# Kernel tuning notes

Hardware: AMD Instinct MI355X
Metric: run time of the kernel (lower is better)

Reference implementation:

```python
import jax, jax.numpy as jnp
import numpy as np
from math import sqrt

B, N, M, HID, NH = 16, 512, 1024, 512, 8
HS = HID // NH  # 64


def layer_norm(x, g, b, eps=1e-5):
    mu = jnp.mean(x, axis=-1, keepdims=True)
    var = jnp.var(x, axis=-1, keepdims=True)
    return (x - mu) * jax.lax.rsqrt(var + eps) * g + b


def apply_moverz(x, s, c):
    # x: [B, L, NH, HS]; s, c: [B, L, 1, HS//2]
    x0, x1 = x[..., 0::2], x[..., 1::2]
    return jnp.concatenate([x0 * c - x1 * s, x1 * c + x0 * s], axis=-1)


def attention(q, k, v, mask):
    # q: [B,Nq,NH,HS], k/v: [B,Nk,NH,HS], mask broadcastable to [B,NH,Nq,Nk]
    attn = jnp.einsum('bnhd,bmhd->bhnm', q, k) / sqrt(HS)
    attn = jnp.where(mask, -jnp.inf, attn)
    attn = jax.nn.softmax(attn, axis=-1)
    x = jnp.einsum('bhnm,bmhd->bnhd', attn, v)
    return x.reshape(x.shape[0], x.shape[1], HID)


def setup_inputs() -> dict:
    key = jax.random.key(0)
    ks = jax.random.split(key, 24)
    inp = {}
    inp['tgt'] = jax.random.normal(ks[0], (B, N, HID), dtype=jnp.float32)
    inp['mem'] = jax.random.normal(ks[1], (B, M, HID), dtype=jnp.float32)
    th_p = jax.random.uniform(ks[2], (B, N, 1, HS // 2), dtype=jnp.float32) * (2 * np.pi)
    th_k = jax.random.uniform(ks[3], (B, M, 1, HS // 2), dtype=jnp.float32) * (2 * np.pi)
    inp['pep_mass_sin'] = jnp.sin(th_p)
    inp['pep_mass_cos'] = jnp.cos(th_p)
    inp['peaks_moverz_sin'] = jnp.sin(th_k)
    inp['peaks_moverz_cos'] = jnp.cos(th_k)
    # causal self-attn mask (True = masked)
    inp['tgt_mask'] = jnp.triu(jnp.ones((N, N), dtype=bool), k=1)[None, None]
    # pad last 64 memory positions
    pad = jnp.arange(M) >= (M - 64)
    inp['mem_key_padding_mask'] = jnp.broadcast_to(pad[None, None, None, :], (B, 1, 1, M))
    s = 0.02
    w = lambda i, shape: jax.random.normal(ks[i], shape, dtype=jnp.float32) * s
    # MaskedMultiHeadAttn params
    inp['mmha_w'] = w(4, (3 * HID, HID)); inp['mmha_b'] = jnp.zeros((3 * HID,), jnp.float32)
    inp['mmha_ow'] = w(5, (HID, HID)); inp['mmha_ob'] = jnp.zeros((HID,), jnp.float32)
    inp['mmha_g'] = jnp.ones((HID,), jnp.float32); inp['mmha_beta'] = jnp.zeros((HID,), jnp.float32)
    # MultiHeadAttn (cross) params
    inp['mha_qw'] = w(6, (HID, HID)); inp['mha_qb'] = jnp.zeros((HID,), jnp.float32)
    inp['mha_kvw'] = w(7, (2 * HID, HID)); inp['mha_kvb'] = jnp.zeros((2 * HID,), jnp.float32)
    inp['mha_ow'] = w(8, (HID, HID)); inp['mha_ob'] = jnp.zeros((HID,), jnp.float32)
    inp['mha_g'] = jnp.ones((HID,), jnp.float32); inp['mha_beta'] = jnp.zeros((HID,), jnp.float32)
    # FFN params (no bias)
    inp['ffn_w1'] = w(9, (4 * HID, HID))
    inp['ffn_w2'] = w(10, (HID, 4 * HID))
    inp['ffn_g'] = jnp.ones((HID,), jnp.float32); inp['ffn_beta'] = jnp.zeros((HID,), jnp.float32)
    return inp


def reference(tgt, mem, pep_mass_sin, pep_mass_cos, peaks_moverz_sin, peaks_moverz_cos,
              tgt_mask, mem_key_padding_mask,
              mmha_w, mmha_b, mmha_ow, mmha_ob, mmha_g, mmha_beta,
              mha_qw, mha_qb, mha_kvw, mha_kvb, mha_ow, mha_ob, mha_g, mha_beta,
              ffn_w1, ffn_w2, ffn_g, ffn_beta):
    # --- masked self-attention ---
    qkv = (tgt @ mmha_w.T + mmha_b).reshape(B, N, NH, 3 * HS)
    q, k, v = jnp.split(qkv, 3, axis=-1)
    x = attention(q, k, v, tgt_mask)
    tgt = layer_norm(x @ mmha_ow.T + mmha_ob + tgt, mmha_g, mmha_beta)
    # --- cross-attention with moverz distance bias ---
    q = (tgt @ mha_qw.T + mha_qb).reshape(B, N, NH, HS)
    q = apply_moverz(q, pep_mass_sin, pep_mass_cos)
    kv = (mem @ mha_kvw.T + mha_kvb).reshape(B, M, NH, 2 * HS)
    k, v = jnp.split(kv, 2, axis=-1)
    k = apply_moverz(k, peaks_moverz_sin, peaks_moverz_cos)
    x = attention(q, k, v, mem_key_padding_mask)
    tgt = layer_norm(x @ mha_ow.T + mha_ob + tgt, mha_g, mha_beta)
    # --- FFN ---
    h = jax.nn.relu(tgt @ ffn_w1.T) @ ffn_w2.T
    tgt = layer_norm(tgt + h, ffn_g, ffn_beta)
    return tgt
```

## Files before the change

kernel.cpp:

```cpp
#include <hip/hip_runtime.h>
#include <hip/hip_bf16.h>

#define BB 16
#define NN 512
#define MM 1024
#define HIDD 512
#define NHH 8

typedef unsigned short ushort_t;
typedef __attribute__((ext_vector_type(8))) short short8;
typedef __attribute__((ext_vector_type(8))) _Float16 half8;
typedef __attribute__((ext_vector_type(4))) _Float16 half4;
typedef __attribute__((ext_vector_type(2))) __fp16 fp16x2;
typedef __attribute__((ext_vector_type(4))) float f32x4;

__device__ __forceinline__ ushort_t f2bf(float x) {
    unsigned u = __float_as_uint(x);
    u += 0x7fff + ((u >> 16) & 1);
    return (ushort_t)(u >> 16);
}

#define GLD16(g, l) __builtin_amdgcn_global_load_lds(                      \
    (const __attribute__((address_space(1))) void*)(g),                    \
    (__attribute__((address_space(3))) void*)(l), 16, 0, 0)


__device__ __forceinline__ void xcd_swizzle(int& colb, int& rowb) {
    int id = blockIdx.x + blockIdx.y * gridDim.x;
    int C = gridDim.x;
    int xcd = id & 7;
    int slot = id >> 3;
    int rows_per = gridDim.y >> 3;
    colb = slot % C;
    rowb = xcd * rows_per + slot / C;
}

__device__ __forceinline__ void xcd_swz_p(int id, int C, int Rdiv8,
                                          int& colb, int& rowb) {
    int xcd = id & 7;
    int slot = id >> 3;
    colb = slot % C;
    rowb = xcd * Rdiv8 + slot / C;
}

__global__ __launch_bounds__(256)
void gemm_bf(const ushort_t* __restrict__ A, const ushort_t* __restrict__ W,
             const float* __restrict__ bias, float* __restrict__ C,
             ushort_t* __restrict__ Cb, _Float16* __restrict__ Ch,
             int K, int Cout, int relu) {
    __shared__ __align__(16) ushort_t smem[2][8192];
    const int tid = threadIdx.x;
    const int lane = tid & 63;
    const int wid = tid >> 6;
    const int wm = wid >> 1, wn = wid & 1;
    int colb, rowb;
    xcd_swizzle(colb, rowb);
    const long row0 = (long)rowb * 128;
    const long col0 = (long)colb * 128;

    const int sr = lane >> 2;
    const int skq = lane & 3;
    const int skx = skq ^ ((sr >> 1) & 3);
    const ushort_t* Ag = A + (row0 + wid * 32 + sr) * (long)K + skx * 8;
    const ushort_t* Wg = W + (col0 + wid * 32 + sr) * (long)K + skx * 8;
    const int sa0 = (wid * 32) * 32, sa1 = (wid * 32 + 16) * 32;

    f32x4 acc[4][4] = {};
    const int lr = lane & 15;
    const int kg = lane >> 4;
    const int kgx = (kg ^ ((lr >> 1) & 3)) * 8;

    GLD16(Ag, &smem[0][sa0]);
    GLD16(Ag + 16 * (long)K, &smem[0][sa1]);
    GLD16(Wg, &smem[0][4096 + sa0]);
    GLD16(Wg + 16 * (long)K, &smem[0][4096 + sa1]);

    int pb = 0;
    for (int k0 = 0; k0 < K; k0 += 32, pb ^= 1) {
        __syncthreads();
        int kn = k0 + 32;
        if (kn < K) {
            GLD16(Ag + kn, &smem[pb ^ 1][sa0]);
            GLD16(Ag + 16 * (long)K + kn, &smem[pb ^ 1][sa1]);
            GLD16(Wg + kn, &smem[pb ^ 1][4096 + sa0]);
            GLD16(Wg + 16 * (long)K + kn, &smem[pb ^ 1][4096 + sa1]);
        }
        const ushort_t* Ab = smem[pb];
        const ushort_t* Wb = smem[pb] + 4096;
        short8 af[4], bfr[4];
#pragma unroll
        for (int i = 0; i < 4; i++)
            af[i] = *(const short8*)&Ab[(wm * 64 + i * 16 + lr) * 32 + kgx];
#pragma unroll
        for (int j = 0; j < 4; j++)
            bfr[j] = *(const short8*)&Wb[(wn * 64 + j * 16 + lr) * 32 + kgx];
#pragma unroll
        for (int i = 0; i < 4; i++)
#pragma unroll
            for (int j = 0; j < 4; j++)
                acc[i][j] = __builtin_amdgcn_mfma_f32_16x16x32_bf16(
                    af[i], bfr[j], acc[i][j], 0, 0, 0);
    }

#pragma unroll
    for (int i = 0; i < 4; i++) {
#pragma unroll
        for (int j = 0; j < 4; j++) {
            long row = row0 + wm * 64 + i * 16 + kg * 4;
            long col = col0 + wn * 64 + j * 16 + lr;
            float bv = bias ? bias[col] : 0.f;
#pragma unroll
            for (int r = 0; r < 4; r++) {
                float x = acc[i][j][r] + bv;
                if (relu) x = fmaxf(x, 0.f);
                size_t idx = (row + r) * (size_t)Cout + col;
                if (Ch)      Ch[idx] = (_Float16)x;
                else if (Cb) Cb[idx] = f2bf(x);
                else         C[idx] = x;
            }
        }
    }
}

__global__ __launch_bounds__(256)
void gemm_qkv_kv(const ushort_t* __restrict__ A, const ushort_t* __restrict__ Wq,
                 const float* __restrict__ bq, _Float16* __restrict__ qkvh,
                 const ushort_t* __restrict__ Mem, const ushort_t* __restrict__ Wkv,
                 const float* __restrict__ bkv,
                 const float* __restrict__ sn, const float* __restrict__ cs,
                 _Float16* __restrict__ Krot, _Float16* __restrict__ Vth) {
    __shared__ __align__(16) ushort_t smem[2][8192];
    const int tid = threadIdx.x;
    const int lane = tid & 63;
    const int wid = tid >> 6;
    const int lr = lane & 15;
    const int kg = lane >> 4;
    const int sr = lane >> 2;
    const int skq = lane & 3;
    const int skx = skq ^ ((sr >> 1) & 3);
    const int kgx = (kg ^ ((lr >> 1) & 3)) * 8;
    const int K = 512;

    if (blockIdx.x < 768) {
        int colb, rowb;
        xcd_swz_p(blockIdx.x, 12, 8, colb, rowb);
        const long row0 = (long)rowb * 128;
        const long col0 = (long)colb * 128;
        const int wm = wid >> 1, wn = wid & 1;
        const ushort_t* Ag = A + (row0 + wid * 32 + sr) * (long)K + skx * 8;
        const ushort_t* Wg = Wq + (col0 + wid * 32 + sr) * (long)K + skx * 8;
        const int sa0 = (wid * 32) * 32, sa1 = (wid * 32 + 16) * 32;

        f32x4 acc[4][4] = {};
        GLD16(Ag, &smem[0][sa0]);
        GLD16(Ag + 16 * (long)K, &smem[0][sa1]);
        GLD16(Wg, &smem[0][4096 + sa0]);
        GLD16(Wg + 16 * (long)K, &smem[0][4096 + sa1]);

        int pb = 0;
        for (int k0 = 0; k0 < K; k0 += 32, pb ^= 1) {
            __syncthreads();
            int kn = k0 + 32;
            if (kn < K) {
                GLD16(Ag + kn, &smem[pb ^ 1][sa0]);
                GLD16(Ag + 16 * (long)K + kn, &smem[pb ^ 1][sa1]);
                GLD16(Wg + kn, &smem[pb ^ 1][4096 + sa0]);
                GLD16(Wg + 16 * (long)K + kn, &smem[pb ^ 1][4096 + sa1]);
            }
            const ushort_t* Ab = smem[pb];
            const ushort_t* Wb = smem[pb] + 4096;
            short8 af[4], bfr[4];
#pragma unroll
            for (int i = 0; i < 4; i++)
                af[i] = *(const short8*)&Ab[(wm * 64 + i * 16 + lr) * 32 + kgx];
#pragma unroll
            for (int j = 0; j < 4; j++)
                bfr[j] = *(const short8*)&Wb[(wn * 64 + j * 16 + lr) * 32 + kgx];
#pragma unroll
            for (int i = 0; i < 4; i++)
#pragma unroll
                for (int j = 0; j < 4; j++)
                    acc[i][j] = __builtin_amdgcn_mfma_f32_16x16x32_bf16(
                        af[i], bfr[j], acc[i][j], 0, 0, 0);
        }

#pragma unroll
        for (int i = 0; i < 4; i++)
#pragma unroll
            for (int j = 0; j < 4; j++) {
                long row = row0 + wm * 64 + i * 16 + kg * 4;
                long col = col0 + wn * 64 + j * 16 + lr;
                float bv = bq[col];
#pragma unroll
                for (int r = 0; r < 4; r++)
                    qkvh[(row + r) * (size_t)1536 + col] =
                        (_Float16)(acc[i][j][r] + bv);
            }
    } else {
        _Float16* Cs = (_Float16*)smem;
        int colb, rowb;
        xcd_swz_p(blockIdx.x - 768, 8, 16, colb, rowb);
        const long row0 = (long)rowb * 128;
        const int h = colb;
        const long col0 = (long)h * 128;
        const int wm = wid >> 1, wn = wid & 1;
        const ushort_t* Ag = Mem + (row0 + wid * 32 + sr) * (long)K + skx * 8;
        const ushort_t* Wg = Wkv + (col0 + wid * 32 + sr) * (long)K + skx * 8;
        const int sa0 = (wid * 32) * 32, sa1 = (wid * 32 + 16) * 32;

        f32x4 acc[4][4] = {};
        GLD16(Ag, &smem[0][sa0]);
        GLD16(Ag + 16 * (long)K, &smem[0][sa1]);
        GLD16(Wg, &smem[0][4096 + sa0]);
        GLD16(Wg + 16 * (long)K, &smem[0][4096 + sa1]);

        int pb = 0;
        for (int k0 = 0; k0 < K; k0 += 32, pb ^= 1) {
            __syncthreads();
            int kn = k0 + 32;
            if (kn < K) {
                GLD16(Ag + kn, &smem[pb ^ 1][sa0]);
                GLD16(Ag + 16 * (long)K + kn, &smem[pb ^ 1][sa1]);
                GLD16(Wg + kn, &smem[pb ^ 1][4096 + sa0]);
                GLD16(Wg + 16 * (long)K + kn, &smem[pb ^ 1][4096 + sa1]);
            }
            const ushort_t* Ab = smem[pb];
            const ushort_t* Wb = smem[pb] + 4096;
            short8 af[4], bfr[4];
#pragma unroll
            for (int i = 0; i < 4; i++)
                af[i] = *(const short8*)&Ab[(wm * 64 + i * 16 + lr) * 32 + kgx];
#pragma unroll
            for (int j = 0; j < 4; j++)
                bfr[j] = *(const short8*)&Wb[(wn * 64 + j * 16 + lr) * 32 + kgx];
#pragma unroll
            for (int i = 0; i < 4; i++)
#pragma unroll
                for (int j = 0; j < 4; j++)
                    acc[i][j] = __builtin_amdgcn_mfma_f32_16x16x32_bf16(
                        af[i], bfr[j], acc[i][j], 0, 0, 0);
        }

        const int b_ = (int)(row0 >> 10);
        const int m0_ = (int)(row0 & 1023);
#pragma unroll
        for (int half = 0; half < 2; half++) {
            __syncthreads();
            if (wn == half) {
#pragma unroll
                for (int i = 0; i < 4; i++)
#pragma unroll
                    for (int j = 0; j < 4; j++) {
                        int row = wm * 64 + i * 16 + kg * 4;
                        int col = j * 16 + lr;
                        float bv = bkv[col0 + half * 64 + col];
#pragma unroll
                        for (int r = 0; r < 4; r++)
                            Cs[(row + r) * 76 + col] = (_Float16)(acc[i][j][r] + bv);
                    }
            }
            __syncthreads();
            if (half == 0) {
                for (int idx = tid; idx < 4096; idx += 256) {
                    int rr = idx >> 5, j = idx & 31;
                    size_t srow = (size_t)row0 + rr;
                    float x0 = (float)Cs[rr * 76 + 2 * j];
                    float x1 = (float)Cs[rr * 76 + 2 * j + 1];
                    float s = sn[srow * 32 + j], c = cs[srow * 32 + j];
                    Krot[srow * 512 + h * 64 + j]      = (_Float16)(x0 * c - x1 * s);
                    Krot[srow * 512 + h * 64 + 32 + j] = (_Float16)(x1 * c + x0 * s);
                }
            } else {
                for (int idx = tid; idx < 1024; idx += 256) {
                    int d = idx >> 4, c = idx & 15;
                    half8 v;
#pragma unroll
                    for (int k = 0; k < 8; k++) v[k] = Cs[(c * 8 + k) * 76 + d];
                    *(half8*)(Vth + (((size_t)(b_ * NHH + h)) * 64 + d) * MM
                              + m0_ + c * 8) = v;
                }
            }
        }
    }
}

__global__ __launch_bounds__(256)
void gemm_bf64(const ushort_t* __restrict__ A, const ushort_t* __restrict__ W,
               const float* __restrict__ bias, float* __restrict__ C,
               ushort_t* __restrict__ Cb, _Float16* __restrict__ Ch,
               int K, int Cout, int relu) {
    __shared__ __align__(16) ushort_t smem[2][6144];
    const int tid = threadIdx.x;
    const int lane = tid & 63;
    const int w = tid >> 6;
    int colb, rowb;
    xcd_swizzle(colb, rowb);
    const long row0 = (long)rowb * 128;
    const long col0 = (long)colb * 64;

    const int sr = lane >> 2;
    const int skq = lane & 3;
    const int skx = skq ^ ((sr >> 1) & 3);
    const ushort_t* Ag = A + (row0 + w * 32 + sr) * (long)K + skx * 8;
    const ushort_t* Wg = W + (col0 + w * 16 + sr) * (long)K + skx * 8;
    const int sa0 = (w * 32) * 32, sa1 = (w * 32 + 16) * 32;
    const int sw0 = 4096 + (w * 16) * 32;

    f32x4 acc[2][4] = {};
    const int lr = lane & 15;
    const int kg = lane >> 4;
    const int kgx = (kg ^ ((lr >> 1) & 3)) * 8;

    GLD16(Ag, &smem[0][sa0]);
    GLD16(Ag + 16 * (long)K, &smem[0][sa1]);
    GLD16(Wg, &smem[0][sw0]);

    int pb = 0;
    for (int k0 = 0; k0 < K; k0 += 32, pb ^= 1) {
        __syncthreads();
        int kn = k0 + 32;
        if (kn < K) {
            GLD16(Ag + kn, &smem[pb ^ 1][sa0]);
            GLD16(Ag + 16 * (long)K + kn, &smem[pb ^ 1][sa1]);
            GLD16(Wg + kn, &smem[pb ^ 1][sw0]);
        }
        const ushort_t* Ab = smem[pb];
        const ushort_t* Wb = smem[pb] + 4096;
        short8 af[2], bfr[4];
#pragma unroll
        for (int i = 0; i < 2; i++)
            af[i] = *(const short8*)&Ab[(w * 32 + i * 16 + lr) * 32 + kgx];
#pragma unroll
        for (int j = 0; j < 4; j++)
            bfr[j] = *(const short8*)&Wb[(j * 16 + lr) * 32 + kgx];
#pragma unroll
        for (int i = 0; i < 2; i++)
#pragma unroll
            for (int j = 0; j < 4; j++)
                acc[i][j] = __builtin_amdgcn_mfma_f32_16x16x32_bf16(
                    af[i], bfr[j], acc[i][j], 0, 0, 0);
    }

#pragma unroll
    for (int i = 0; i < 2; i++) {
#pragma unroll
        for (int j = 0; j < 4; j++) {
            long row = row0 + w * 32 + i * 16 + kg * 4;
            long col = col0 + j * 16 + lr;
            float bv = bias ? bias[col] : 0.f;
#pragma unroll
            for (int r = 0; r < 4; r++) {
                float x = acc[i][j][r] + bv;
                if (relu) x = fmaxf(x, 0.f);
                size_t idx = (row + r) * (size_t)Cout + col;
                if (Ch)      Ch[idx] = (_Float16)x;
                else if (Cb) Cb[idx] = f2bf(x);
                else         C[idx] = x;
            }
        }
    }
}

__global__ __launch_bounds__(256)
void gemm_bf64_sk(const ushort_t* __restrict__ A, const ushort_t* __restrict__ W,
                  int lda, int Kslice, float* __restrict__ C0,
                  float* __restrict__ C1, int Cout) {
    __shared__ __align__(16) ushort_t smem[2][6144];
    const int tid = threadIdx.x;
    const int lane = tid & 63;
    const int w = tid >> 6;
    int colb, rowb;
    xcd_swizzle(colb, rowb);
    const long row0 = (long)rowb * 128;
    const long col0 = (long)colb * 64;
    const long koff = (long)blockIdx.z * Kslice;
    float* __restrict__ C = blockIdx.z ? C1 : C0;

    const int sr = lane >> 2;
    const int skq = lane & 3;
    const int skx = skq ^ ((sr >> 1) & 3);
    const ushort_t* Ag = A + (row0 + w * 32 + sr) * (long)lda + koff + skx * 8;
    const ushort_t* Wg = W + (col0 + w * 16 + sr) * (long)lda + koff + skx * 8;
    const int sa0 = (w * 32) * 32, sa1 = (w * 32 + 16) * 32;
    const int sw0 = 4096 + (w * 16) * 32;

    f32x4 acc[2][4] = {};
    const int lr = lane & 15;
    const int kg = lane >> 4;
    const int kgx = (kg ^ ((lr >> 1) & 3)) * 8;

    GLD16(Ag, &smem[0][sa0]);
    GLD16(Ag + 16 * (long)lda, &smem[0][sa1]);
    GLD16(Wg, &smem[0][sw0]);

    int pb = 0;
    for (int k0 = 0; k0 < Kslice; k0 += 32, pb ^= 1) {
        __syncthreads();
        int kn = k0 + 32;
        if (kn < Kslice) {
            GLD16(Ag + kn, &smem[pb ^ 1][sa0]);
            GLD16(Ag + 16 * (long)lda + kn, &smem[pb ^ 1][sa1]);
            GLD16(Wg + kn, &smem[pb ^ 1][sw0]);
        }
        const ushort_t* Ab = smem[pb];
        const ushort_t* Wb = smem[pb] + 4096;
        short8 af[2], bfr[4];
#pragma unroll
        for (int i = 0; i < 2; i++)
            af[i] = *(const short8*)&Ab[(w * 32 + i * 16 + lr) * 32 + kgx];
#pragma unroll
        for (int j = 0; j < 4; j++)
            bfr[j] = *(const short8*)&Wb[(j * 16 + lr) * 32 + kgx];
#pragma unroll
        for (int i = 0; i < 2; i++)
#pragma unroll
            for (int j = 0; j < 4; j++)
                acc[i][j] = __builtin_amdgcn_mfma_f32_16x16x32_bf16(
                    af[i], bfr[j], acc[i][j], 0, 0, 0);
    }

#pragma unroll
    for (int i = 0; i < 2; i++)
#pragma unroll
        for (int j = 0; j < 4; j++) {
            long row = row0 + w * 32 + i * 16 + kg * 4;
            long col = col0 + j * 16 + lr;
#pragma unroll
            for (int r = 0; r < 4; r++)
                C[(row + r) * (size_t)Cout + col] = acc[i][j][r];
        }
}

__global__ __launch_bounds__(256)
void gemm_q_rot(const ushort_t* __restrict__ A, const ushort_t* __restrict__ W,
                const float* __restrict__ bias,
                const float* __restrict__ sn, const float* __restrict__ cs,
                _Float16* __restrict__ Qrot) {
    __shared__ __align__(16) ushort_t smem[2][6144];
    _Float16* Cs = (_Float16*)smem;
    const int K = 512;
    const int tid = threadIdx.x;
    const int lane = tid & 63;
    const int w = tid >> 6;
    int colb, rowb;
    xcd_swizzle(colb, rowb);
    const long row0 = (long)rowb * 128;
    const int h = colb;
    const long col0 = (long)h * 64;

    const int sr = lane >> 2;
    const int skq = lane & 3;
    const int skx = skq ^ ((sr >> 1) & 3);
    const ushort_t* Ag = A + (row0 + w * 32 + sr) * (long)K + skx * 8;
    const ushort_t* Wg = W + (col0 + w * 16 + sr) * (long)K + skx * 8;
    const int sa0 = (w * 32) * 32, sa1 = (w * 32 + 16) * 32;
    const int sw0 = 4096 + (w * 16) * 32;

    f32x4 acc[2][4] = {};
    const int lr = lane & 15;
    const int kg = lane >> 4;
    const int kgx = (kg ^ ((lr >> 1) & 3)) * 8;

    GLD16(Ag, &smem[0][sa0]);
    GLD16(Ag + 16 * (long)K, &smem[0][sa1]);
    GLD16(Wg, &smem[0][sw0]);

    int pb = 0;
    for (int k0 = 0; k0 < K; k0 += 32, pb ^= 1) {
        __syncthreads();
        int kn = k0 + 32;
        if (kn < K) {
            GLD16(Ag + kn, &smem[pb ^ 1][sa0]);
            GLD16(Ag + 16 * (long)K + kn, &smem[pb ^ 1][sa1]);
            GLD16(Wg + kn, &smem[pb ^ 1][sw0]);
        }
        const ushort_t* Ab = smem[pb];
        const ushort_t* Wb = smem[pb] + 4096;
        short8 af[2], bfr[4];
#pragma unroll
        for (int i = 0; i < 2; i++)
            af[i] = *(const short8*)&Ab[(w * 32 + i * 16 + lr) * 32 + kgx];
#pragma unroll
        for (int j = 0; j < 4; j++)
            bfr[j] = *(const short8*)&Wb[(j * 16 + lr) * 32 + kgx];
#pragma unroll
        for (int i = 0; i < 2; i++)
#pragma unroll
            for (int j = 0; j < 4; j++)
                acc[i][j] = __builtin_amdgcn_mfma_f32_16x16x32_bf16(
                    af[i], bfr[j], acc[i][j], 0, 0, 0);
    }

    __syncthreads();
#pragma unroll
    for (int i = 0; i < 2; i++)
#pragma unroll
        for (int j = 0; j < 4; j++) {
            int row = w * 32 + i * 16 + kg * 4;
            int col = j * 16 + lr;
            float bv = bias[col0 + col];
#pragma unroll
            for (int r = 0; r < 4; r++)
                Cs[(row + r) * 76 + col] = (_Float16)(acc[i][j][r] + bv);
        }
    __syncthreads();
    for (int idx = tid; idx < 4096; idx += 256) {
        int rr = idx >> 5, j = idx & 31;
        size_t srow = (size_t)row0 + rr;
        float x0 = (float)Cs[rr * 76 + 2 * j], x1 = (float)Cs[rr * 76 + 2 * j + 1];
        float s = sn[srow * 32 + j], c = cs[srow * 32 + j];
        Qrot[srow * 512 + h * 64 + j]      = (_Float16)(x0 * c - x1 * s);
        Qrot[srow * 512 + h * 64 + 32 + j] = (_Float16)(x1 * c + x0 * s);
    }
}

__global__ __launch_bounds__(256)
void cvt_all(const float* __restrict__ tgt, const float* __restrict__ mem,
             const float* __restrict__ w0, const float* __restrict__ w1,
             const float* __restrict__ w2, const float* __restrict__ w3,
             const float* __restrict__ w4, const float* __restrict__ w5,
             const float* __restrict__ w6,
             ushort_t* __restrict__ Abf, ushort_t* __restrict__ membf,
             ushort_t* __restrict__ Wbf) {
    int blk = blockIdx.x;
    const float* src;
    ushort_t* dst;
    size_t off;
    if (blk < 4096)       { src = tgt; dst = Abf;   off = (size_t)blk * 1024; }
    else if (blk < 12288) { src = mem; dst = membf; off = (size_t)(blk - 4096) * 1024; }
    else {
        int wb = blk - 12288;
        dst = Wbf + (size_t)wb * 1024;
        if (wb < 768)       { src = w0; off = (size_t)wb * 1024; }
        else if (wb < 1024) { src = w1; off = (size_t)(wb - 768) * 1024; }
        else if (wb < 1280) { src = w2; off = (size_t)(wb - 1024) * 1024; }
        else if (wb < 1792) { src = w3; off = (size_t)(wb - 1280) * 1024; }
        else if (wb < 2048) { src = w4; off = (size_t)(wb - 1792) * 1024; }
        else if (wb < 3072) { src = w5; off = (size_t)(wb - 2048) * 1024; }
        else                { src = w6; off = (size_t)(wb - 3072) * 1024; }
        float4 v = *(const float4*)(src + off + threadIdx.x * 4);
        ushort4 o;
        o.x = f2bf(v.x); o.y = f2bf(v.y); o.z = f2bf(v.z); o.w = f2bf(v.w);
        *(ushort4*)(dst + threadIdx.x * 4) = o;
        return;
    }
    float4 v = *(const float4*)(src + off + threadIdx.x * 4);
    ushort4 o;
    o.x = f2bf(v.x); o.y = f2bf(v.y); o.z = f2bf(v.z); o.w = f2bf(v.w);
    *(ushort4*)(dst + off + threadIdx.x * 4) = o;
}

__global__ __launch_bounds__(256)
void prep_vt(const _Float16* __restrict__ src, int L, int stride,
             int hmul, int hadd, _Float16* __restrict__ Vt) {
    const int b = blockIdx.z, h = blockIdx.y, m0 = blockIdx.x * 64;
    const int tid = threadIdx.x;
    __shared__ _Float16 vt[64][72];
    for (int idx = tid; idx < 512; idx += 256) {
        int m = idx >> 3, c = idx & 7;
        half8 v = *(const half8*)(src + ((size_t)(b * L + m0 + m)) * stride
                                  + h * hmul + hadd + c * 8);
#pragma unroll
        for (int k = 0; k < 8; k++) vt[c * 8 + k][m] = v[k];
    }
    __syncthreads();
    for (int idx = tid; idx < 512; idx += 256) {
        int d = idx >> 3, c = idx & 7;
        *(half8*)(Vt + (((size_t)(b * NHH + h)) * 64 + d) * L + m0 + c * 8)
            = *(const half8*)&vt[d][c * 8];
    }
}

__global__ __launch_bounds__(256, 4)
void attn11(const _Float16* __restrict__ Q, int qstride, int qmul, int qadd,
            const _Float16* __restrict__ K, int kstride, int kmul, int kadd,
            const _Float16* __restrict__ Vt, int LV, int Lrows,
            ushort_t* __restrict__ out, int kvlen, int causal) {
    const int g = blockIdx.x;
    const int bh = (g & 7) * 16 + ((g >> 3) & 15);
    const int qraw = g >> 7;
    const int qb = causal ? ((0x12476530u >> (qraw << 2)) & 7) : qraw;
    const int b = bh >> 3, h = bh & 7;
    const int n0 = qb * 64;
    const int tid = threadIdx.x, lane = tid & 63, w = tid >> 6;
    const int quad = lane >> 4, l16 = lane & 15;
    const int qw = n0 + w * 16;

    __shared__ _Float16 Ks[2][64 * 64];
    __shared__ _Float16 Vs[2][64 * 64];
    __shared__ _Float16 Ps[4][16 * 64];
    _Float16* Pw = Ps[w];

    half8 bq[2];
#pragma unroll
    for (int c = 0; c < 2; c++)
        bq[c] = *(const half8*)(Q + ((size_t)(b * NN + qw + l16)) * qstride
                                + h * qmul + qadd + c * 32 + quad * 8);

    f32x4 acc[4] = {};
    float mrun = -3e38f, lrun = 0.f;

    const int srow = tid >> 3;
    const int scol = tid & 7;
    const int ssw = (scol ^ (srow & 7)) * 8;

    const int limit = causal ? (n0 + 64) : kvlen;
    const int nt = limit >> 6;

    const size_t kbase = ((size_t)(b * Lrows)) * kstride + h * kmul + kadd;
    const size_t vbase = (((size_t)(b * NHH + h)) * 64 + srow) * (size_t)LV;

    half8 kr0, kr1, vr0, vr1;
    {
        size_t kb = kbase + (size_t)srow * kstride + scol * 8;
        kr0 = *(const half8*)(K + kb);
        kr1 = *(const half8*)(K + kb + (size_t)32 * kstride);
        vr0 = *(const half8*)(Vt + vbase + scol * 8);
        vr1 = *(const half8*)(Vt + vbase + (size_t)32 * LV + scol * 8);
    }
    *(half8*)&Ks[0][srow * 64 + ssw] = kr0;
    *(half8*)&Ks[0][(srow + 32) * 64 + ssw] = kr1;
    *(half8*)&Vs[0][srow * 64 + ssw] = vr0;
    *(half8*)&Vs[0][(srow + 32) * 64 + ssw] = vr1;
    if (nt > 1) {
        size_t kb = kbase + (size_t)(64 + srow) * kstride + scol * 8;
        kr0 = *(const half8*)(K + kb);
        kr1 = *(const half8*)(K + kb + (size_t)32 * kstride);
        vr0 = *(const half8*)(Vt + vbase + 64 + scol * 8);
        vr1 = *(const half8*)(Vt + vbase + (size_t)32 * LV + 64 + scol * 8);
    }

    const float SC = 0.125f * 1.44269504f;
    const int fsw = l16 & 7;
    int pb = 0;
    for (int t = 0; t < nt; t++, pb ^= 1) {
        const int key0 = t * 64;
        __syncthreads();
        if (t + 1 < nt) {
            *(half8*)&Ks[pb ^ 1][srow * 64 + ssw] = kr0;
            *(half8*)&Ks[pb ^ 1][(srow + 32) * 64 + ssw] = kr1;
            *(half8*)&Vs[pb ^ 1][srow * 64 + ssw] = vr0;
            *(half8*)&Vs[pb ^ 1][(srow + 32) * 64 + ssw] = vr1;
            if (t + 2 < nt) {
                size_t kb = kbase + (size_t)((t + 2) * 64 + srow) * kstride + scol * 8;
                kr0 = *(const half8*)(K + kb);
                kr1 = *(const half8*)(K + kb + (size_t)32 * kstride);
                vr0 = *(const half8*)(Vt + vbase + (t + 2) * 64 + scol * 8);
                vr1 = *(const half8*)(Vt + vbase + (size_t)32 * LV
                                      + (t + 2) * 64 + scol * 8);
            }
        }

        const _Float16* Kb = Ks[pb];
        const _Float16* Vb = Vs[pb];
        f32x4 st[4];
        __builtin_amdgcn_s_setprio(1);
#pragma unroll
        for (int kt = 0; kt < 4; kt++) {
            const int rk = kt * 16 + l16;
            half8 ak0 = *(const half8*)&Kb[rk * 64 + ((quad ^ fsw) * 8)];
            half8 ak1 = *(const half8*)&Kb[rk * 64 + (((quad + 4) ^ fsw) * 8)];
            f32x4 z = {};
            z = __builtin_amdgcn_mfma_f32_16x16x32_f16(ak0, bq[0], z, 0, 0, 0);
            z = __builtin_amdgcn_mfma_f32_16x16x32_f16(ak1, bq[1], z, 0, 0, 0);
            st[kt] = z;
        }
        __builtin_amdgcn_s_setprio(0);

        if (causal && key0 + 64 > qw) {
            const int qabs = qw + l16;
#pragma unroll
            for (int kt = 0; kt < 4; kt++)
#pragma unroll
                for (int r = 0; r < 4; r++)
                    if (key0 + kt * 16 + quad * 4 + r > qabs)
                        st[kt][r] = -3e38f;
        }

        float plm = -3e38f;
#pragma unroll
        for (int kt = 0; kt < 4; kt++)
            plm = fmaxf(plm, fmaxf(fmaxf(st[kt][0], st[kt][1]),
                                   fmaxf(st[kt][2], st[kt][3])));

        const int keep = __all(plm - mrun <= 64.f);
        if (!keep) {
            float lm = fmaxf(plm, __shfl_xor(plm, 16));
            lm = fmaxf(lm, __shfl_xor(lm, 32));
            float mnew = fmaxf(mrun, lm);
            float corr = exp2f((mrun - mnew) * SC);
            mrun = mnew;
            lrun *= corr;
            float cb0 = __shfl(corr, (lane & 48) | (quad * 4 + 0));
            float cb1 = __shfl(corr, (lane & 48) | (quad * 4 + 1));
            float cb2 = __shfl(corr, (lane & 48) | (quad * 4 + 2));
            float cb3 = __shfl(corr, (lane & 48) | (quad * 4 + 3));
#pragma unroll
            for (int dt = 0; dt < 4; dt++) {
                acc[dt][0] *= cb0; acc[dt][1] *= cb1;
                acc[dt][2] *= cb2; acc[dt][3] *= cb3;
            }
        }
        const float mb = mrun * SC;
#pragma unroll
        for (int kt = 0; kt < 4; kt++) {
            float p0 = exp2f(__builtin_fmaf(st[kt][0], SC, -mb));
            float p1 = exp2f(__builtin_fmaf(st[kt][1], SC, -mb));
            float p2 = exp2f(__builtin_fmaf(st[kt][2], SC, -mb));
            float p3 = exp2f(__builtin_fmaf(st[kt][3], SC, -mb));
            lrun += (p0 + p1) + (p2 + p3);
            fp16x2 lo = __builtin_amdgcn_cvt_pkrtz(p0, p1);
            fp16x2 hi = __builtin_amdgcn_cvt_pkrtz(p2, p3);
            union { unsigned u[2]; half4 h; } pk;
            pk.u[0] = __builtin_bit_cast(unsigned, lo);
            pk.u[1] = __builtin_bit_cast(unsigned, hi);
            int jc = 2 * kt + (quad >> 1);
            *(half4*)&Pw[l16 * 64 + ((jc ^ fsw) * 8) + (quad & 1) * 4] = pk.h;
        }
        half8 ap[2];
#pragma unroll
        for (int c = 0; c < 2; c++)
            ap[c] = *(const half8*)&Pw[l16 * 64 + (((c * 4 + quad) ^ fsw) * 8)];
        __builtin_amdgcn_s_setprio(1);
#pragma unroll
        for (int dt = 0; dt < 4; dt++) {
            const int rv = dt * 16 + l16;
            half8 bv0 = *(const half8*)&Vb[rv * 64 + ((quad ^ fsw) * 8)];
            half8 bv1 = *(const half8*)&Vb[rv * 64 + (((quad + 4) ^ fsw) * 8)];
            acc[dt] = __builtin_amdgcn_mfma_f32_16x16x32_f16(ap[0], bv0, acc[dt], 0, 0, 0);
            acc[dt] = __builtin_amdgcn_mfma_f32_16x16x32_f16(ap[1], bv1, acc[dt], 0, 0, 0);
        }
        __builtin_amdgcn_s_setprio(0);
    }

    lrun += __shfl_xor(lrun, 16);
    lrun += __shfl_xor(lrun, 32);
    float invq = 1.f / lrun;
    float iv0 = __shfl(invq, (lane & 48) | (quad * 4 + 0));
    float iv1 = __shfl(invq, (lane & 48) | (quad * 4 + 1));
    float iv2 = __shfl(invq, (lane & 48) | (quad * 4 + 2));
    float iv3 = __shfl(invq, (lane & 48) | (quad * 4 + 3));
#pragma unroll
    for (int dt = 0; dt < 4; dt++) {
        size_t base = ((size_t)(b * NN + qw + quad * 4)) * 512
                      + h * 64 + dt * 16 + l16;
        out[base]           = f2bf(acc[dt][0] * iv0);
        out[base + 512]     = f2bf(acc[dt][1] * iv1);
        out[base + 1024]    = f2bf(acc[dt][2] * iv2);
        out[base + 1536]    = f2bf(acc[dt][3] * iv3);
    }
}

__global__ __launch_bounds__(256)
void ln_residual(const float* __restrict__ u, const float* __restrict__ u2,
                 const float* __restrict__ res,
                 const float* __restrict__ g, const float* __restrict__ be,
                 float* __restrict__ out, ushort_t* __restrict__ outbf) {
    const int row = blockIdx.x, t = threadIdx.x;
    const float* rp = res + (size_t)row * HIDD;
    const float* up = u + (size_t)row * HIDD;
    float z0 = rp[t] + up[t];
    float z1 = rp[t + 256] + up[t + 256];
    if (u2) {
        const float* up2 = u2 + (size_t)row * HIDD;
        z0 += up2[t];
        z1 += up2[t + 256];
    }
    float sm = z0 + z1, s2 = z0 * z0 + z1 * z1;
#pragma unroll
    for (int off = 1; off < 64; off <<= 1) {
        sm += __shfl_xor(sm, off, 64);
        s2 += __shfl_xor(s2, off, 64);
    }
    __shared__ float ps[4], ps2[4];
    int w = t >> 6;
    if ((t & 63) == 0) { ps[w] = sm; ps2[w] = s2; }
    __syncthreads();
    sm = ps[0] + ps[1] + ps[2] + ps[3];
    s2 = ps2[0] + ps2[1] + ps2[2] + ps2[3];
    float mu = sm * (1.f / 512.f);
    float var = s2 * (1.f / 512.f) - mu * mu;
    float rstd = rsqrtf(var + 1e-5f);
    float y0 = (z0 - mu) * rstd * g[t] + be[t];
    float y1 = (z1 - mu) * rstd * g[t + 256] + be[t + 256];
    out[(size_t)row * HIDD + t]       = y0;
    out[(size_t)row * HIDD + t + 256] = y1;
    if (outbf) {
        outbf[(size_t)row * HIDD + t]       = f2bf(y0);
        outbf[(size_t)row * HIDD + t + 256] = f2bf(y1);
    }
}

extern "C" void kernel_launch(void* const* d_in, const int* in_sizes, int n_in,
                              void* d_out, int out_size, void* d_ws, size_t ws_size,
                              hipStream_t stream) {
    const float* tgt      = (const float*)d_in[0];
    const float* mem      = (const float*)d_in[1];
    const float* pep_sin  = (const float*)d_in[2];
    const float* pep_cos  = (const float*)d_in[3];
    const float* pk_sin   = (const float*)d_in[4];
    const float* pk_cos   = (const float*)d_in[5];
    const float* mmha_w   = (const float*)d_in[8];
    const float* mmha_b   = (const float*)d_in[9];
    const float* mmha_ow  = (const float*)d_in[10];
    const float* mmha_ob  = (const float*)d_in[11];
    const float* mmha_g   = (const float*)d_in[12];
    const float* mmha_be  = (const float*)d_in[13];
    const float* mha_qw   = (const float*)d_in[14];
    const float* mha_qb   = (const float*)d_in[15];
    const float* mha_kvw  = (const float*)d_in[16];
    const float* mha_kvb  = (const float*)d_in[17];
    const float* mha_ow   = (const float*)d_in[18];
    const float* mha_ob   = (const float*)d_in[19];
    const float* mha_g    = (const float*)d_in[20];
    const float* mha_be   = (const float*)d_in[21];
    const float* ffn_w1   = (const float*)d_in[22];
    const float* ffn_w2   = (const float*)d_in[23];
    const float* ffn_g    = (const float*)d_in[24];
    const float* ffn_be   = (const float*)d_in[25];

    float* ws = (float*)d_ws;
    float* utmp  = ws;
    float* tgt12 = ws + 4194304;
    _Float16* hp = (_Float16*)(ws + 8388608);
    _Float16* qkvh  = hp;
    _Float16* Qrot  = hp + 12582912;
    _Float16* Vth   = hp + 16777216;
    _Float16* Krot  = hp + 25165824;
    ushort_t* membf = (ushort_t*)(hp + 33554432);
    ushort_t* Abf   = (ushort_t*)(hp + 41943040);
    ushort_t* Wbf   = (ushort_t*)(hp + 46137344);
    ushort_t* w_mmha = Wbf;
    ushort_t* w_mmow = Wbf + 786432;
    ushort_t* w_qw   = Wbf + 1048576;
    ushort_t* w_kvw  = Wbf + 1310720;
    ushort_t* w_mow  = Wbf + 1835008;
    ushort_t* w_f1   = Wbf + 2097152;
    ushort_t* w_f2   = Wbf + 3145728;
    _Float16* Vth_self = hp + 50331648;
    ushort_t* hbf = (ushort_t*)qkvh;
    float* utmp2 = (float*)Krot;
    float* out = (float*)d_out;
    (void)in_sizes; (void)n_in; (void)out_size; (void)ws_size;

    cvt_all<<<16384, 256, 0, stream>>>(tgt, mem, mmha_w, mmha_ow, mha_qw,
                                       mha_kvw, mha_ow, ffn_w1, ffn_w2,
                                       Abf, membf, Wbf);
    gemm_qkv_kv<<<1792, 256, 0, stream>>>(Abf, w_mmha, mmha_b, qkvh,
                                          membf, w_kvw, mha_kvb,
                                          pk_sin, pk_cos, Krot, Vth);
    prep_vt<<<dim3(8, NHH, BB), 256, 0, stream>>>(qkvh, NN, 1536, 192, 128, Vth_self);
    attn11<<<1024, 256, 0, stream>>>(qkvh, 1536, 192, 0, qkvh, 1536, 192, 64,
                                     Vth_self, NN, NN, Abf, 0, 1);
    gemm_bf64<<<dim3(8, 64), 256, 0, stream>>>(Abf, w_mmow, mmha_ob, utmp, nullptr, nullptr, 512, 512, 0);
    ln_residual<<<8192, 256, 0, stream>>>(utmp, nullptr, tgt, mmha_g, mmha_be, tgt12, Abf);
    gemm_q_rot<<<dim3(8, 64), 256, 0, stream>>>(Abf, w_qw, mha_qb, pep_sin, pep_cos, Qrot);
    attn11<<<1024, 256, 0, stream>>>(Qrot, 512, 64, 0, Krot, 512, 64, 0,
                                     Vth, MM, MM, Abf, MM - 64, 0);
    gemm_bf64<<<dim3(8, 64), 256, 0, stream>>>(Abf, w_mow, mha_ob, utmp, nullptr, nullptr, 512, 512, 0);
    ln_residual<<<8192, 256, 0, stream>>>(utmp, nullptr, tgt12, mha_g, mha_be, tgt12, Abf);
    gemm_bf<<<dim3(16, 64), 256, 0, stream>>>(Abf, w_f1, nullptr, nullptr, hbf, nullptr, 512, 2048, 1);
    gemm_bf64_sk<<<dim3(8, 64, 2), 256, 0, stream>>>(hbf, w_f2, 2048, 1024, utmp, utmp2, 512);
    ln_residual<<<8192, 256, 0, stream>>>(utmp, utmp2, tgt12, ffn_g, ffn_be, out, nullptr);
}
```

Before: 397.0 us.

## Triple-buffer LDS in GEMM kernels with explicit vmcnt-based waits

Every GEMM main loop moves from a double-buffered shared-memory pipeline to a three-stage ring. Each stage prefetches two K-tiles ahead and replaces `__syncthreads` with an inline `s_waitcnt vmcnt(N)` plus `s_barrier`, so one tile's loads stay in flight while the current tile is computed. The goal is to hide more global-to-LDS latency behind the MFMA work. The cost is 50% more shared memory per block, which may reduce occupancy. Near the end of the loop, redundant clamped loads are issued. In `gemm_q_rot` and the KV branch these pending loads are not explicitly drained before the shared buffer is reused, which may race.

```diff
diff --git a/kernel.cpp b/kernel.cpp
--- a/kernel.cpp
+++ b/kernel.cpp
@@ -23,6 +23,7 @@
 #define GLD16(g, l) __builtin_amdgcn_global_load_lds(                      \
     (const __attribute__((address_space(1))) void*)(g),                    \
     (__attribute__((address_space(3))) void*)(l), 16, 0, 0)
+
 
 
 __device__ __forceinline__ void xcd_swizzle(int& colb, int& rowb) {
@@ -48,7 +49,7 @@
              const float* __restrict__ bias, float* __restrict__ C,
              ushort_t* __restrict__ Cb, _Float16* __restrict__ Ch,
              int K, int Cout, int relu) {
-    __shared__ __align__(16) ushort_t smem[2][8192];
+    __shared__ __align__(16) ushort_t smem[3][8192];
     const int tid = threadIdx.x;
     const int lane = tid & 63;
     const int wid = tid >> 6;
@@ -70,23 +71,31 @@
     const int kg = lane >> 4;
     const int kgx = (kg ^ ((lr >> 1) & 3)) * 8;
 
+    const int nt = K >> 5;
     GLD16(Ag, &smem[0][sa0]);
     GLD16(Ag + 16 * (long)K, &smem[0][sa1]);
     GLD16(Wg, &smem[0][4096 + sa0]);
     GLD16(Wg + 16 * (long)K, &smem[0][4096 + sa1]);
-
-    int pb = 0;
-    for (int k0 = 0; k0 < K; k0 += 32, pb ^= 1) {
-        __syncthreads();
-        int kn = k0 + 32;
-        if (kn < K) {
-            GLD16(Ag + kn, &smem[pb ^ 1][sa0]);
-            GLD16(Ag + 16 * (long)K + kn, &smem[pb ^ 1][sa1]);
-            GLD16(Wg + kn, &smem[pb ^ 1][4096 + sa0]);
-            GLD16(Wg + 16 * (long)K + kn, &smem[pb ^ 1][4096 + sa1]);
-        }
-        const ushort_t* Ab = smem[pb];
-        const ushort_t* Wb = smem[pb] + 4096;
+    GLD16(Ag + 32, &smem[1][sa0]);
+    GLD16(Ag + 16 * (long)K + 32, &smem[1][sa1]);
+    GLD16(Wg + 32, &smem[1][4096 + sa0]);
+    GLD16(Wg + 16 * (long)K + 32, &smem[1][4096 + sa1]);
+
+    int cur = 0;
+    for (int t = 0; t < nt; t++) {
+        asm volatile("s_waitcnt vmcnt(4)\n\ts_barrier" ::: "memory");
+        __builtin_amdgcn_sched_barrier(0);
+        {
+            int nxt = (t + 2 < nt) ? t + 2 : nt - 1;
+            int nb = cur + 2; if (nb >= 3) nb -= 3;
+            long kk = (long)nxt << 5;
+            GLD16(Ag + kk, &smem[nb][sa0]);
+            GLD16(Ag + 16 * (long)K + kk, &smem[nb][sa1]);
+            GLD16(Wg + kk, &smem[nb][4096 + sa0]);
+            GLD16(Wg + 16 * (long)K + kk, &smem[nb][4096 + sa1]);
+        }
+        const ushort_t* Ab = smem[cur];
+        const ushort_t* Wb = smem[cur] + 4096;
         short8 af[4], bfr[4];
 #pragma unroll
         for (int i = 0; i < 4; i++)
@@ -100,7 +109,9 @@
             for (int j = 0; j < 4; j++)
                 acc[i][j] = __builtin_amdgcn_mfma_f32_16x16x32_bf16(
                     af[i], bfr[j], acc[i][j], 0, 0, 0);
-    }
+        cur = (cur == 2) ? 0 : cur + 1;
+    }
+    asm volatile("s_waitcnt vmcnt(0)" ::: "memory");
 
 #pragma unroll
     for (int i = 0; i < 4; i++) {
@@ -129,7 +140,7 @@
                  const float* __restrict__ bkv,
                  const float* __restrict__ sn, const float* __restrict__ cs,
                  _Float16* __restrict__ Krot, _Float16* __restrict__ Vth) {
-    __shared__ __align__(16) ushort_t smem[2][8192];
+    __shared__ __align__(16) ushort_t smem[3][8192];
     const int tid = threadIdx.x;
     const int lane = tid & 63;
     const int wid = tid >> 6;
@@ -140,6 +151,7 @@
     const int skx = skq ^ ((sr >> 1) & 3);
     const int kgx = (kg ^ ((lr >> 1) & 3)) * 8;
     const int K = 512;
+    const int nt = 16;
 
     if (blockIdx.x < 768) {
         int colb, rowb;
@@ -156,19 +168,26 @@
         GLD16(Ag + 16 * (long)K, &smem[0][sa1]);
         GLD16(Wg, &smem[0][4096 + sa0]);
         GLD16(Wg + 16 * (long)K, &smem[0][4096 + sa1]);
-
-        int pb = 0;
-        for (int k0 = 0; k0 < K; k0 += 32, pb ^= 1) {
-            __syncthreads();
-            int kn = k0 + 32;
-            if (kn < K) {
-                GLD16(Ag + kn, &smem[pb ^ 1][sa0]);
-                GLD16(Ag + 16 * (long)K + kn, &smem[pb ^ 1][sa1]);
-                GLD16(Wg + kn, &smem[pb ^ 1][4096 + sa0]);
-                GLD16(Wg + 16 * (long)K + kn, &smem[pb ^ 1][4096 + sa1]);
+        GLD16(Ag + 32, &smem[1][sa0]);
+        GLD16(Ag + 16 * (long)K + 32, &smem[1][sa1]);
+        GLD16(Wg + 32, &smem[1][4096 + sa0]);
+        GLD16(Wg + 16 * (long)K + 32, &smem[1][4096 + sa1]);
+
+        int cur = 0;
+        for (int t = 0; t < nt; t++) {
+            asm volatile("s_waitcnt vmcnt(4)\n\ts_barrier" ::: "memory");
+            __builtin_amdgcn_sched_barrier(0);
+            {
+                int nxt = (t + 2 < nt) ? t + 2 : nt - 1;
+                int nb = cur + 2; if (nb >= 3) nb -= 3;
+                long kk = (long)nxt << 5;
+                GLD16(Ag + kk, &smem[nb][sa0]);
+                GLD16(Ag + 16 * (long)K + kk, &smem[nb][sa1]);
+                GLD16(Wg + kk, &smem[nb][4096 + sa0]);
+                GLD16(Wg + 16 * (long)K + kk, &smem[nb][4096 + sa1]);
             }
-            const ushort_t* Ab = smem[pb];
-            const ushort_t* Wb = smem[pb] + 4096;
+            const ushort_t* Ab = smem[cur];
+            const ushort_t* Wb = smem[cur] + 4096;
             short8 af[4], bfr[4];
 #pragma unroll
             for (int i = 0; i < 4; i++)
@@ -182,7 +201,9 @@
                 for (int j = 0; j < 4; j++)
                     acc[i][j] = __builtin_amdgcn_mfma_f32_16x16x32_bf16(
                         af[i], bfr[j], acc[i][j], 0, 0, 0);
-        }
+            cur = (cur == 2) ? 0 : cur + 1;
+        }
+        asm volatile("s_waitcnt vmcnt(0)" ::: "memory");
 
 #pragma unroll
         for (int i = 0; i < 4; i++)
@@ -213,19 +234,26 @@
         GLD16(Ag + 16 * (long)K, &smem[0][sa1]);
         GLD16(Wg, &smem[0][4096 + sa0]);
         GLD16(Wg + 16 * (long)K, &smem[0][4096 + sa1]);
-
-        int pb = 0;
-        for (int k0 = 0; k0 < K; k0 += 32, pb ^= 1) {
-            __syncthreads();
-            int kn = k0 + 32;
-            if (kn < K) {
-                GLD16(Ag + kn, &smem[pb ^ 1][sa0]);
-                GLD16(Ag + 16 * (long)K + kn, &smem[pb ^ 1][sa1]);
-                GLD16(Wg + kn, &smem[pb ^ 1][4096 + sa0]);
-                GLD16(Wg + 16 * (long)K + kn, &smem[pb ^ 1][4096 + sa1]);
+        GLD16(Ag + 32, &smem[1][sa0]);
+        GLD16(Ag + 16 * (long)K + 32, &smem[1][sa1]);
+        GLD16(Wg + 32, &smem[1][4096 + sa0]);
+        GLD16(Wg + 16 * (long)K + 32, &smem[1][4096 + sa1]);
+
+        int cur = 0;
+        for (int t = 0; t < nt; t++) {
+            asm volatile("s_waitcnt vmcnt(4)\n\ts_barrier" ::: "memory");
+            __builtin_amdgcn_sched_barrier(0);
+            {
+                int nxt = (t + 2 < nt) ? t + 2 : nt - 1;
+                int nb = cur + 2; if (nb >= 3) nb -= 3;
+                long kk = (long)nxt << 5;
+                GLD16(Ag + kk, &smem[nb][sa0]);
+                GLD16(Ag + 16 * (long)K + kk, &smem[nb][sa1]);
+                GLD16(Wg + kk, &smem[nb][4096 + sa0]);
+                GLD16(Wg + 16 * (long)K + kk, &smem[nb][4096 + sa1]);
             }
-            const ushort_t* Ab = smem[pb];
-            const ushort_t* Wb = smem[pb] + 4096;
+            const ushort_t* Ab = smem[cur];
+            const ushort_t* Wb = smem[cur] + 4096;
             short8 af[4], bfr[4];
 #pragma unroll
             for (int i = 0; i < 4; i++)
@@ -239,6 +267,7 @@
                 for (int j = 0; j < 4; j++)
                     acc[i][j] = __builtin_amdgcn_mfma_f32_16x16x32_bf16(
                         af[i], bfr[j], acc[i][j], 0, 0, 0);
+            cur = (cur == 2) ? 0 : cur + 1;
         }
 
         const int b_ = (int)(row0 >> 10);
@@ -289,7 +318,7 @@
                const float* __restrict__ bias, float* __restrict__ C,
                ushort_t* __restrict__ Cb, _Float16* __restrict__ Ch,
                int K, int Cout, int relu) {
-    __shared__ __align__(16) ushort_t smem[2][6144];
+    __shared__ __align__(16) ushort_t smem[3][6144];
     const int tid = threadIdx.x;
     const int lane = tid & 63;
     const int w = tid >> 6;
@@ -311,21 +340,28 @@
     const int kg = lane >> 4;
     const int kgx = (kg ^ ((lr >> 1) & 3)) * 8;
 
+    const int nt = K >> 5;
     GLD16(Ag, &smem[0][sa0]);
     GLD16(Ag + 16 * (long)K, &smem[0][sa1]);
     GLD16(Wg, &smem[0][sw0]);
-
-    int pb = 0;
-    for (int k0 = 0; k0 < K; k0 += 32, pb ^= 1) {
-        __syncthreads();
-        int kn = k0 + 32;
-        if (kn < K) {
-            GLD16(Ag + kn, &smem[pb ^ 1][sa0]);
-            GLD16(Ag + 16 * (long)K + kn, &smem[pb ^ 1][sa1]);
-            GLD16(Wg + kn, &smem[pb ^ 1][sw0]);
-        }
-        const ushort_t* Ab = smem[pb];
-        const ushort_t* Wb = smem[pb] + 4096;
+    GLD16(Ag + 32, &smem[1][sa0]);
+    GLD16(Ag + 16 * (long)K + 32, &smem[1][sa1]);
+    GLD16(Wg + 32, &smem[1][sw0]);
+
+    int cur = 0;
+    for (int t = 0; t < nt; t++) {
+        asm volatile("s_waitcnt vmcnt(3)\n\ts_barrier" ::: "memory");
+        __builtin_amdgcn_sched_barrier(0);
+        {
+            int nxt = (t + 2 < nt) ? t + 2 : nt - 1;
+            int nb = cur + 2; if (nb >= 3) nb -= 3;
+            long kk = (long)nxt << 5;
+            GLD16(Ag + kk, &smem[nb][sa0]);
+            GLD16(Ag + 16 * (long)K + kk, &smem[nb][sa1]);
+            GLD16(Wg + kk, &smem[nb][sw0]);
+        }
+        const ushort_t* Ab = smem[cur];
+        const ushort_t* Wb = smem[cur] + 4096;
         short8 af[2], bfr[4];
 #pragma unroll
         for (int i = 0; i < 2; i++)
@@ -339,7 +375,9 @@
             for (int j = 0; j < 4; j++)
                 acc[i][j] = __builtin_amdgcn_mfma_f32_16x16x32_bf16(
                     af[i], bfr[j], acc[i][j], 0, 0, 0);
-    }
+        cur = (cur == 2) ? 0 : cur + 1;
+    }
+    asm volatile("s_waitcnt vmcnt(0)" ::: "memory");
 
 #pragma unroll
     for (int i = 0; i < 2; i++) {
@@ -365,7 +403,7 @@
 void gemm_bf64_sk(const ushort_t* __restrict__ A, const ushort_t* __restrict__ W,
                   int lda, int Kslice, float* __restrict__ C0,
                   float* __restrict__ C1, int Cout) {
-    __shared__ __align__(16) ushort_t smem[2][6144];
+    __shared__ __align__(16) ushort_t smem[3][6144];
     const int tid = threadIdx.x;
     const int lane = tid & 63;
     const int w = tid >> 6;
@@ -389,21 +427,28 @@
     const int kg = lane >> 4;
     const int kgx = (kg ^ ((lr >> 1) & 3)) * 8;
 
+    const int nt = Kslice >> 5;
     GLD16(Ag, &smem[0][sa0]);
     GLD16(Ag + 16 * (long)lda, &smem[0][sa1]);
     GLD16(Wg, &smem[0][sw0]);
-
-    int pb = 0;
-    for (int k0 = 0; k0 < Kslice; k0 += 32, pb ^= 1) {
-        __syncthreads();
-        int kn = k0 + 32;
-        if (kn < Kslice) {
-            GLD16(Ag + kn, &smem[pb ^ 1][sa0]);
-            GLD16(Ag + 16 * (long)lda + kn, &smem[pb ^ 1][sa1]);
-            GLD16(Wg + kn, &smem[pb ^ 1][sw0]);
-        }
-        const ushort_t* Ab = smem[pb];
-        const ushort_t* Wb = smem[pb] + 4096;
+    GLD16(Ag + 32, &smem[1][sa0]);
+    GLD16(Ag + 16 * (long)lda + 32, &smem[1][sa1]);
+    GLD16(Wg + 32, &smem[1][sw0]);
+
+    int cur = 0;
+    for (int t = 0; t < nt; t++) {
+        asm volatile("s_waitcnt vmcnt(3)\n\ts_barrier" ::: "memory");
+        __builtin_amdgcn_sched_barrier(0);
+        {
+            int nxt = (t + 2 < nt) ? t + 2 : nt - 1;
+            int nb = cur + 2; if (nb >= 3) nb -= 3;
+            long kk = (long)nxt << 5;
+            GLD16(Ag + kk, &smem[nb][sa0]);
+            GLD16(Ag + 16 * (long)lda + kk, &smem[nb][sa1]);
+            GLD16(Wg + kk, &smem[nb][sw0]);
+        }
+        const ushort_t* Ab = smem[cur];
+        const ushort_t* Wb = smem[cur] + 4096;
         short8 af[2], bfr[4];
 #pragma unroll
         for (int i = 0; i < 2; i++)
@@ -417,7 +462,9 @@
             for (int j = 0; j < 4; j++)
                 acc[i][j] = __builtin_amdgcn_mfma_f32_16x16x32_bf16(
                     af[i], bfr[j], acc[i][j], 0, 0, 0);
-    }
+        cur = (cur == 2) ? 0 : cur + 1;
+    }
+    asm volatile("s_waitcnt vmcnt(0)" ::: "memory");
 
 #pragma unroll
     for (int i = 0; i < 2; i++)
@@ -436,7 +483,7 @@
                 const float* __restrict__ bias,
                 const float* __restrict__ sn, const float* __restrict__ cs,
                 _Float16* __restrict__ Qrot) {
-    __shared__ __align__(16) ushort_t smem[2][6144];
+    __shared__ __align__(16) ushort_t smem[3][6144];
     _Float16* Cs = (_Float16*)smem;
     const int K = 512;
     const int tid = threadIdx.x;
@@ -461,21 +508,28 @@
     const int kg = lane >> 4;
     const int kgx = (kg ^ ((lr >> 1) & 3)) * 8;
 
+    const int nt = K >> 5;
     GLD16(Ag, &smem[0][sa0]);
     GLD16(Ag + 16 * (long)K, &smem[0][sa1]);
     GLD16(Wg, &smem[0][sw0]);
-
-    int pb = 0;
-    for (int k0 = 0; k0 < K; k0 += 32, pb ^= 1) {
-        __syncthreads();
-        int kn = k0 + 32;
-        if (kn < K) {
-            GLD16(Ag + kn, &smem[pb ^ 1][sa0]);
-            GLD16(Ag + 16 * (long)K + kn, &smem[pb ^ 1][sa1]);
-            GLD16(Wg + kn, &smem[pb ^ 1][sw0]);
-        }
-        const ushort_t* Ab = smem[pb];
-        const ushort_t* Wb = smem[pb] + 4096;
+    GLD16(Ag + 32, &smem[1][sa0]);
+    GLD16(Ag + 16 * (long)K + 32, &smem[1][sa1]);
+    GLD16(Wg + 32, &smem[1][sw0]);
+
+    int cur = 0;
+    for (int t = 0; t < nt; t++) {
+        asm volatile("s_waitcnt vmcnt(3)\n\ts_barrier" ::: "memory");
+        __builtin_amdgcn_sched_barrier(0);
+        {
+            int nxt = (t + 2 < nt) ? t + 2 : nt - 1;
+            int nb = cur + 2; if (nb >= 3) nb -= 3;
+            long kk = (long)nxt << 5;
+            GLD16(Ag + kk, &smem[nb][sa0]);
+            GLD16(Ag + 16 * (long)K + kk, &smem[nb][sa1]);
+            GLD16(Wg + kk, &smem[nb][sw0]);
+        }
+        const ushort_t* Ab = smem[cur];
+        const ushort_t* Wb = smem[cur] + 4096;
         short8 af[2], bfr[4];
 #pragma unroll
         for (int i = 0; i < 2; i++)
@@ -489,6 +543,7 @@
             for (int j = 0; j < 4; j++)
                 acc[i][j] = __builtin_amdgcn_mfma_f32_16x16x32_bf16(
                     af[i], bfr[j], acc[i][j], 0, 0, 0);
+        cur = (cur == 2) ? 0 : cur + 1;
     }
 
     __syncthreads();
```

Result: slower. 406.3 us (+2.3%).
